# Kernel tuning notes

Measured on AMD Instinct MI355X. Metric: run time of the kernel, lower is better.

## Reference

```python
import jax, jax.numpy as jnp
import numpy as np

B, T, L, D, U = 2048, 500, 128, 64, 128  # batch, time steps, latent_dim, output_dim, n_units


def setup_inputs() -> dict:
    key = jax.random.key(0)
    ks = jax.random.split(key, 10)
    def init(k, shape, fan_in):
        return jax.random.uniform(k, shape, jnp.float32, -1.0, 1.0) / np.sqrt(fan_in)
    return {
        "first_point": jax.random.normal(ks[0], (1, B, L), jnp.float32),
        "time_steps_to_predict": jnp.arange(T, dtype=jnp.float32),
        # GRUCell params (torch layout: weight [3*hidden, in], gates ordered r,z,n)
        "w_ih": init(ks[1], (3 * L, D + 1), L),
        "w_hh": init(ks[2], (3 * L, L), L),
        "b_ih": init(ks[3], (3 * L,), L),
        "b_hh": init(ks[4], (3 * L,), L),
        # output_net: Linear(L,U) -> tanh -> Linear(U,D)
        "w1": init(ks[5], (U, L), L),
        "b1": jnp.zeros((U,), jnp.float32),
        "w2": init(ks[6], (D, U), U),
        "b2": jnp.zeros((D,), jnp.float32),
    }


def _gru_cell(x, h, w_ih, w_hh, b_ih, b_hh):
    gi = x @ w_ih.T + b_ih  # [B, 3L]
    gh = h @ w_hh.T + b_hh  # [B, 3L]
    i_r, i_z, i_n = jnp.split(gi, 3, axis=-1)
    h_r, h_z, h_n = jnp.split(gh, 3, axis=-1)
    r = jax.nn.sigmoid(i_r + h_r)
    z = jax.nn.sigmoid(i_z + h_z)
    n = jnp.tanh(i_n + r * h_n)
    return (1.0 - z) * n + z * h


def reference(first_point, time_steps_to_predict, w_ih, w_hh, b_ih, b_hh, w1, b1, w2, b2):
    def mlp(h):
        return jnp.tanh(h @ w1.T + b1) @ w2.T + b2  # [B, D]

    ts = time_steps_to_predict
    delta_ts = jnp.concatenate([jnp.zeros((1,), ts.dtype), ts[1:] - ts[:-1]])  # [T]

    h0 = first_point[0]          # [B, L]
    p0 = mlp(h0)                 # [B, D]
    batch = h0.shape[0]

    def step(carry, dt):
        h, p = carry
        dt_col = jnp.broadcast_to(dt.reshape(1, 1), (batch, 1))
        x = jnp.concatenate([p, dt_col], axis=-1)  # [B, D+1]
        h = _gru_cell(x, h, w_ih, w_hh, b_ih, b_hh)
        p = mlp(h)
        return (h, p), (h, p)

    _, (hs, ps) = jax.lax.scan(step, (h0, p0), delta_ts[1:])  # [T-1, B, *]
    sol_z = jnp.concatenate([h0[None], hs], axis=0)   # [T, B, L]
    pred_x = jnp.concatenate([p0[None], ps], axis=0)  # [T, B, D]
    sol_z = jnp.transpose(sol_z, (1, 0, 2))[None]     # [1, B, T, L]
    pred_x = jnp.transpose(pred_x, (1, 0, 2))[None]   # [1, B, T, D]
    return sol_z, pred_x
```

## Files before the change

### kernel.cpp

```cpp
#include <hip/hip_runtime.h>

#define BB 2048
#define TT 500
#define LL 128
#define DD 64
#define UU 128

using f16x8 = __attribute__((ext_vector_type(8))) _Float16;
using f32x4 = __attribute__((ext_vector_type(4))) float;

__device__ __forceinline__ float bf2f(unsigned short u){
  union { unsigned u; float f; } v; v.u = ((unsigned)u) << 16; return v.f;
}
__device__ __forceinline__ unsigned short f2bf(float f){
  union { float f; unsigned u; } v; v.f = f;
  unsigned r = v.u + 0x7FFFu + ((v.u >> 16) & 1u);
  return (unsigned short)(r >> 16);
}
__device__ __forceinline__ float cvt(unsigned short v){ return bf2f(v); }
__device__ __forceinline__ float cvt(float v){ return v; }

__device__ __forceinline__ float sigmoidf_(float x){
  return __builtin_amdgcn_rcpf(1.f + __expf(-x));
}
__device__ __forceinline__ float tanhf_(float x){
  float e = __expf(2.f * x);
  return 1.f - 2.f * __builtin_amdgcn_rcpf(1.f + e);
}

#define SH 136
#define SP 72
#define SA 136

struct Frags {
  f16x8 Wp[3][2];
  f16x8 Wh[3][4];
  f16x8 W1f[4];
  f16x8 W2f[4];
  float br, bz, bin, bhn, wdr, wdz, wdn, b1c, b2c;
};

template <typename T>
__device__ __forceinline__ void preload(
    const void* wih_, const void* whh_, const void* bih_, const void* bhh_,
    const void* w1_, const void* b1_, const void* w2_, const void* b2_,
    int c, int lq, Frags& F)
{
  const T* wih = (const T*)wih_; const T* whh = (const T*)whh_;
  const T* bih = (const T*)bih_; const T* bhh = (const T*)bhh_;
  const T* w1  = (const T*)w1_;  const T* b1  = (const T*)b1_;
  const T* w2  = (const T*)w2_;  const T* b2  = (const T*)b2_;
  #pragma unroll
  for (int g = 0; g < 3; ++g){
    const int row = g*128 + c;
    #pragma unroll
    for (int kt = 0; kt < 2; ++kt)
      #pragma unroll
      for (int j = 0; j < 8; ++j)
        F.Wp[g][kt][j] = (_Float16)cvt(wih[row*65 + kt*32 + lq*8 + j]);
    #pragma unroll
    for (int kt = 0; kt < 4; ++kt)
      #pragma unroll
      for (int j = 0; j < 8; ++j)
        F.Wh[g][kt][j] = (_Float16)cvt(whh[row*128 + kt*32 + lq*8 + j]);
  }
  #pragma unroll
  for (int kt = 0; kt < 4; ++kt)
    #pragma unroll
    for (int j = 0; j < 8; ++j)
      F.W1f[kt][j] = (_Float16)cvt(w1[c*128 + kt*32 + lq*8 + j]);
  const int c2 = c & 63;
  #pragma unroll
  for (int kt = 0; kt < 4; ++kt)
    #pragma unroll
    for (int j = 0; j < 8; ++j)
      F.W2f[kt][j] = (_Float16)cvt(w2[c2*128 + kt*32 + lq*8 + j]);
  F.br  = cvt(bih[c])     + cvt(bhh[c]);
  F.bz  = cvt(bih[128+c]) + cvt(bhh[128+c]);
  F.bin = cvt(bih[256+c]);
  F.bhn = cvt(bhh[256+c]);
  F.wdr = cvt(wih[c*65 + 64]);
  F.wdz = cvt(wih[(128+c)*65 + 64]);
  F.wdn = cvt(wih[(256+c)*65 + 64]);
  F.b1c = cvt(b1[c]);
  F.b2c = cvt(b2[c2]);
}

__global__ __launch_bounds__(512, 2) void rnn_decoder(
    const void* __restrict__ fp0,
    const void* __restrict__ ts,
    const void* __restrict__ wih,
    const void* __restrict__ whh,
    const void* __restrict__ bih,
    const void* __restrict__ bhh,
    const void* __restrict__ w1,
    const void* __restrict__ b1,
    const void* __restrict__ w2,
    const void* __restrict__ b2,
    void* __restrict__ out)
{
  __shared__ __align__(16) _Float16 sh[16*SH];
  __shared__ __align__(16) _Float16 sp[16*SP];
  __shared__ __align__(16) _Float16 sa[16*SA];
  __shared__ float dts[TT];

  const int tid  = threadIdx.x;
  const int wv   = tid >> 6;
  const int lane = tid & 63;
  const int lm   = lane & 15;
  const int lq   = lane >> 4;
  const int b0   = blockIdx.x << 4;
  const int c    = (wv << 4) + lm;

  const bool isbf = (((const unsigned*)ts)[1] != 0x3F800000u);

  for (int i = tid; i < 16*SH; i += 512) sh[i] = (_Float16)0.f;
  for (int i = tid; i < 16*SP; i += 512) sp[i] = (_Float16)0.f;
  for (int i = tid; i < 16*SA; i += 512) sa[i] = (_Float16)0.f;

  Frags F;
  if (isbf) preload<unsigned short>(wih, whh, bih, bhh, w1, b1, w2, b2, c, lq, F);
  else      preload<float>         (wih, whh, bih, bhh, w1, b1, w2, b2, c, lq, F);

  if (isbf){
    const unsigned short* t16 = (const unsigned short*)ts;
    for (int t = tid; t < TT; t += 512)
      dts[t] = t ? (bf2f(t16[t]) - bf2f(t16[t-1])) : 0.f;
  } else {
    const float* t32 = (const float*)ts;
    for (int t = tid; t < TT; t += 512)
      dts[t] = t ? (t32[t] - t32[t-1]) : 0.f;
  }

  {
    const int row = tid >> 5;
    const int k4  = (tid & 31) << 2;
    if (isbf){
      const unsigned short* src = (const unsigned short*)fp0 + (b0 + row)*LL + k4;
      #pragma unroll
      for (int j = 0; j < 4; ++j) sh[row*SH + k4 + j] = (_Float16)bf2f(src[j]);
    } else {
      const float* src = (const float*)fp0 + (b0 + row)*LL + k4;
      #pragma unroll
      for (int j = 0; j < 4; ++j) sh[row*SH + k4 + j] = (_Float16)src[j];
    }
  }
  __syncthreads();

  float hprev[4];
  #pragma unroll
  for (int i = 0; i < 4; ++i)
    hprev[i] = (float)sh[(lq*4 + i)*SH + c];

  unsigned short* outh16 = (unsigned short*)out;
  unsigned short* outp16 = outh16 + (size_t)BB*TT*LL;
  float* outh32 = (float*)out;
  float* outp32 = outh32 + (size_t)BB*TT*LL;

  for (int t = 0; t < TT; ++t){
    if (t > 0){
      const float dt = dts[t];
      f16x8 ap[2], ah[4];
      #pragma unroll
      for (int kt = 0; kt < 2; ++kt)
        ap[kt] = *(const f16x8*)&sp[lm*SP + kt*32 + lq*8];
      #pragma unroll
      for (int kt = 0; kt < 4; ++kt)
        ah[kt] = *(const f16x8*)&sh[lm*SH + kt*32 + lq*8];
      f32x4 aR = {0,0,0,0}, aZ = {0,0,0,0}, aN = {0,0,0,0}, aH = {0,0,0,0};
      #pragma unroll
      for (int kt = 0; kt < 2; ++kt){
        aR = __builtin_amdgcn_mfma_f32_16x16x32_f16(ap[kt], F.Wp[0][kt], aR, 0,0,0);
        aZ = __builtin_amdgcn_mfma_f32_16x16x32_f16(ap[kt], F.Wp[1][kt], aZ, 0,0,0);
        aN = __builtin_amdgcn_mfma_f32_16x16x32_f16(ap[kt], F.Wp[2][kt], aN, 0,0,0);
      }
      #pragma unroll
      for (int kt = 0; kt < 4; ++kt){
        aR = __builtin_amdgcn_mfma_f32_16x16x32_f16(ah[kt], F.Wh[0][kt], aR, 0,0,0);
        aZ = __builtin_amdgcn_mfma_f32_16x16x32_f16(ah[kt], F.Wh[1][kt], aZ, 0,0,0);
        aH = __builtin_amdgcn_mfma_f32_16x16x32_f16(ah[kt], F.Wh[2][kt], aH, 0,0,0);
      }
      float hnew[4];
      #pragma unroll
      for (int i = 0; i < 4; ++i){
        const float r = sigmoidf_(aR[i] + F.br + dt*F.wdr);
        const float z = sigmoidf_(aZ[i] + F.bz + dt*F.wdz);
        const float n = tanhf_(aN[i] + F.bin + dt*F.wdn + r*(aH[i] + F.bhn));
        hnew[i] = (1.f - z)*n + z*hprev[i];
        hprev[i] = hnew[i];
      }
      __syncthreads();
      #pragma unroll
      for (int i = 0; i < 4; ++i)
        sh[(lq*4 + i)*SH + c] = (_Float16)hnew[i];
      __syncthreads();
    }
    {
      f16x8 ahm[4];
      #pragma unroll
      for (int kt = 0; kt < 4; ++kt)
        ahm[kt] = *(const f16x8*)&sh[lm*SH + kt*32 + lq*8];
      f32x4 acc = {0,0,0,0};
      #pragma unroll
      for (int kt = 0; kt < 4; ++kt)
        acc = __builtin_amdgcn_mfma_f32_16x16x32_f16(ahm[kt], F.W1f[kt], acc, 0,0,0);
      #pragma unroll
      for (int i = 0; i < 4; ++i)
        sa[(lq*4 + i)*SA + c] = (_Float16)tanhf_(acc[i] + F.b1c);
    }
    __syncthreads();
    if (wv < 4){
      f16x8 aam[4];
      #pragma unroll
      for (int kt = 0; kt < 4; ++kt)
        aam[kt] = *(const f16x8*)&sa[lm*SA + kt*32 + lq*8];
      f32x4 acc = {0,0,0,0};
      #pragma unroll
      for (int kt = 0; kt < 4; ++kt)
        acc = __builtin_amdgcn_mfma_f32_16x16x32_f16(aam[kt], F.W2f[kt], acc, 0,0,0);
      #pragma unroll
      for (int i = 0; i < 4; ++i)
        sp[(lq*4 + i)*SP + c] = (_Float16)(acc[i] + F.b2c);
    }
    __syncthreads();
    {
      const int row = tid >> 5;
      const size_t hb = (size_t)(b0 + row)*TT + t;
      const int k4 = (tid & 31) << 2;
      const int k2 = (tid & 31) << 1;
      if (isbf){
        ushort4 hv;
        hv.x = f2bf((float)sh[row*SH + k4 + 0]);
        hv.y = f2bf((float)sh[row*SH + k4 + 1]);
        hv.z = f2bf((float)sh[row*SH + k4 + 2]);
        hv.w = f2bf((float)sh[row*SH + k4 + 3]);
        *(ushort4*)(outh16 + hb*LL + k4) = hv;
        ushort2 pv;
        pv.x = f2bf((float)sp[row*SP + k2 + 0]);
        pv.y = f2bf((float)sp[row*SP + k2 + 1]);
        *(ushort2*)(outp16 + hb*DD + k2) = pv;
      } else {
        float4 hv;
        hv.x = (float)sh[row*SH + k4 + 0];
        hv.y = (float)sh[row*SH + k4 + 1];
        hv.z = (float)sh[row*SH + k4 + 2];
        hv.w = (float)sh[row*SH + k4 + 3];
        *(float4*)(outh32 + hb*LL + k4) = hv;
        float2 pv;
        pv.x = (float)sp[row*SP + k2 + 0];
        pv.y = (float)sp[row*SP + k2 + 1];
        *(float2*)(outp32 + hb*DD + k2) = pv;
      }
    }
  }
}

extern "C" void kernel_launch(void* const* d_in, const int* in_sizes, int n_in,
                              void* d_out, int out_size, void* d_ws, size_t ws_size,
                              hipStream_t stream) {
  (void)in_sizes; (void)n_in; (void)out_size; (void)d_ws; (void)ws_size;
  rnn_decoder<<<dim3(BB/16), dim3(512), 0, stream>>>(
      d_in[0],
      d_in[1],
      d_in[2],
      d_in[3],
      d_in[4],
      d_in[5],
      d_in[6],
      d_in[7],
      d_in[8],
      d_in[9],
      d_out);
}
```

Baseline: 1.444 ms.

## Fold output projection into GRU input weights and write outputs directly from registers

Precomputes Wc = W_ih[:, :64] @ W2 and a folded bias so the GRU input gates take the tanh activation directly, dropping the p staging buffer and one barrier phase per step. The p output is computed alongside the gates, off the critical path. h and p are now stored straight from MFMA registers to global memory instead of being re-read from shared memory. Costs are an O(64) per-thread prologue loop, extra MFMAs per step (K=128 instead of 64 for the input part), and scattered element-wise global stores that replace the vectorized ones.

```diff
diff --git a/kernel.cpp b/kernel.cpp
--- a/kernel.cpp
+++ b/kernel.cpp
@@ -29,11 +29,10 @@
 }
 
 #define SH 136
-#define SP 72
 #define SA 136
 
 struct Frags {
-  f16x8 Wp[3][2];
+  f16x8 Wc[3][4];
   f16x8 Wh[3][4];
   f16x8 W1f[4];
   f16x8 W2f[4];
@@ -54,11 +53,6 @@
   for (int g = 0; g < 3; ++g){
     const int row = g*128 + c;
     #pragma unroll
-    for (int kt = 0; kt < 2; ++kt)
-      #pragma unroll
-      for (int j = 0; j < 8; ++j)
-        F.Wp[g][kt][j] = (_Float16)cvt(wih[row*65 + kt*32 + lq*8 + j]);
-    #pragma unroll
     for (int kt = 0; kt < 4; ++kt)
       #pragma unroll
       for (int j = 0; j < 8; ++j)
@@ -75,9 +69,41 @@
     #pragma unroll
     for (int j = 0; j < 8; ++j)
       F.W2f[kt][j] = (_Float16)cvt(w2[c2*128 + kt*32 + lq*8 + j]);
-  F.br  = cvt(bih[c])     + cvt(bhh[c]);
-  F.bz  = cvt(bih[128+c]) + cvt(bhh[128+c]);
-  F.bin = cvt(bih[256+c]);
+
+  for (int kt = 0; kt < 4; ++kt){
+    float acc[3][8];
+    #pragma unroll
+    for (int g = 0; g < 3; ++g)
+      #pragma unroll
+      for (int j = 0; j < 8; ++j) acc[g][j] = 0.f;
+    for (int d = 0; d < 64; ++d){
+      float w2r[8];
+      #pragma unroll
+      for (int j = 0; j < 8; ++j)
+        w2r[j] = cvt(w2[d*128 + kt*32 + lq*8 + j]);
+      #pragma unroll
+      for (int g = 0; g < 3; ++g){
+        const float wpv = cvt(wih[(g*128 + c)*65 + d]);
+        #pragma unroll
+        for (int j = 0; j < 8; ++j) acc[g][j] += wpv * w2r[j];
+      }
+    }
+    #pragma unroll
+    for (int g = 0; g < 3; ++g)
+      #pragma unroll
+      for (int j = 0; j < 8; ++j)
+        F.Wc[g][kt][j] = (_Float16)acc[g][j];
+  }
+  float bc[3] = {0.f, 0.f, 0.f};
+  for (int d = 0; d < 64; ++d){
+    const float b2v = cvt(b2[d]);
+    #pragma unroll
+    for (int g = 0; g < 3; ++g)
+      bc[g] += cvt(wih[(g*128 + c)*65 + d]) * b2v;
+  }
+  F.br  = cvt(bih[c])     + cvt(bhh[c])     + bc[0];
+  F.bz  = cvt(bih[128+c]) + cvt(bhh[128+c]) + bc[1];
+  F.bin = cvt(bih[256+c]) + bc[2];
   F.bhn = cvt(bhh[256+c]);
   F.wdr = cvt(wih[c*65 + 64]);
   F.wdz = cvt(wih[(128+c)*65 + 64]);
@@ -100,7 +126,6 @@
     void* __restrict__ out)
 {
   __shared__ __align__(16) _Float16 sh[16*SH];
-  __shared__ __align__(16) _Float16 sp[16*SP];
   __shared__ __align__(16) _Float16 sa[16*SA];
   __shared__ float dts[TT];
 
@@ -113,10 +138,6 @@
   const int c    = (wv << 4) + lm;
 
   const bool isbf = (((const unsigned*)ts)[1] != 0x3F800000u);
-
-  for (int i = tid; i < 16*SH; i += 512) sh[i] = (_Float16)0.f;
-  for (int i = tid; i < 16*SP; i += 512) sp[i] = (_Float16)0.f;
-  for (int i = tid; i < 16*SA; i += 512) sa[i] = (_Float16)0.f;
 
   Frags F;
   if (isbf) preload<unsigned short>(wih, whh, bih, bhh, w1, b1, w2, b2, c, lq, F);
@@ -132,17 +153,29 @@
       dts[t] = t ? (t32[t] - t32[t-1]) : 0.f;
   }
 
+  unsigned short* outh16 = (unsigned short*)out;
+  unsigned short* outp16 = outh16 + (size_t)BB*TT*LL;
+  float* outh32 = (float*)out;
+  float* outp32 = outh32 + (size_t)BB*TT*LL;
+
   {
     const int row = tid >> 5;
     const int k4  = (tid & 31) << 2;
     if (isbf){
       const unsigned short* src = (const unsigned short*)fp0 + (b0 + row)*LL + k4;
-      #pragma unroll
-      for (int j = 0; j < 4; ++j) sh[row*SH + k4 + j] = (_Float16)bf2f(src[j]);
+      ushort4 v = *(const ushort4*)src;
+      #pragma unroll
+      for (int j = 0; j < 4; ++j)
+        sh[row*SH + k4 + j] = (_Float16)bf2f(((const unsigned short*)&v)[j]);
+      *(ushort4*)(outh16 + (size_t)(b0 + row)*TT*LL + k4) = v;
     } else {
       const float* src = (const float*)fp0 + (b0 + row)*LL + k4;
-      #pragma unroll
-      for (int j = 0; j < 4; ++j) sh[row*SH + k4 + j] = (_Float16)src[j];
+      float4 v = *(const float4*)src;
+      sh[row*SH + k4 + 0] = (_Float16)v.x;
+      sh[row*SH + k4 + 1] = (_Float16)v.y;
+      sh[row*SH + k4 + 2] = (_Float16)v.z;
+      sh[row*SH + k4 + 3] = (_Float16)v.w;
+      *(float4*)(outh32 + (size_t)(b0 + row)*TT*LL + k4) = v;
     }
   }
   __syncthreads();
@@ -152,105 +185,109 @@
   for (int i = 0; i < 4; ++i)
     hprev[i] = (float)sh[(lq*4 + i)*SH + c];
 
-  unsigned short* outh16 = (unsigned short*)out;
-  unsigned short* outp16 = outh16 + (size_t)BB*TT*LL;
-  float* outh32 = (float*)out;
-  float* outp32 = outh32 + (size_t)BB*TT*LL;
-
-  for (int t = 0; t < TT; ++t){
-    if (t > 0){
-      const float dt = dts[t];
-      f16x8 ap[2], ah[4];
-      #pragma unroll
-      for (int kt = 0; kt < 2; ++kt)
-        ap[kt] = *(const f16x8*)&sp[lm*SP + kt*32 + lq*8];
+  f16x8 ahc[4], aac[4];
+  #pragma unroll
+  for (int kt = 0; kt < 4; ++kt)
+    ahc[kt] = *(const f16x8*)&sh[lm*SH + kt*32 + lq*8];
+
+  {
+    f32x4 acc = {0,0,0,0};
+    #pragma unroll
+    for (int kt = 0; kt < 4; ++kt)
+      acc = __builtin_amdgcn_mfma_f32_16x16x32_f16(ahc[kt], F.W1f[kt], acc, 0,0,0);
+    #pragma unroll
+    for (int i = 0; i < 4; ++i)
+      sa[(lq*4 + i)*SA + c] = (_Float16)tanhf_(acc[i] + F.b1c);
+  }
+  __syncthreads();
+  #pragma unroll
+  for (int kt = 0; kt < 4; ++kt)
+    aac[kt] = *(const f16x8*)&sa[lm*SA + kt*32 + lq*8];
+
+  for (int t = 1; t < TT; ++t){
+    const float dt = dts[t];
+    f32x4 aR = {0,0,0,0}, aZ = {0,0,0,0}, aN = {0,0,0,0}, aH = {0,0,0,0};
+    #pragma unroll
+    for (int kt = 0; kt < 4; ++kt){
+      aR = __builtin_amdgcn_mfma_f32_16x16x32_f16(aac[kt], F.Wc[0][kt], aR, 0,0,0);
+      aZ = __builtin_amdgcn_mfma_f32_16x16x32_f16(aac[kt], F.Wc[1][kt], aZ, 0,0,0);
+      aN = __builtin_amdgcn_mfma_f32_16x16x32_f16(aac[kt], F.Wc[2][kt], aN, 0,0,0);
+      aH = __builtin_amdgcn_mfma_f32_16x16x32_f16(ahc[kt], F.Wh[2][kt], aH, 0,0,0);
+    }
+    #pragma unroll
+    for (int kt = 0; kt < 4; ++kt){
+      aR = __builtin_amdgcn_mfma_f32_16x16x32_f16(ahc[kt], F.Wh[0][kt], aR, 0,0,0);
+      aZ = __builtin_amdgcn_mfma_f32_16x16x32_f16(ahc[kt], F.Wh[1][kt], aZ, 0,0,0);
+    }
+    f32x4 aP = {0,0,0,0};
+    if (wv < 4){
       #pragma unroll
       for (int kt = 0; kt < 4; ++kt)
-        ah[kt] = *(const f16x8*)&sh[lm*SH + kt*32 + lq*8];
-      f32x4 aR = {0,0,0,0}, aZ = {0,0,0,0}, aN = {0,0,0,0}, aH = {0,0,0,0};
-      #pragma unroll
-      for (int kt = 0; kt < 2; ++kt){
-        aR = __builtin_amdgcn_mfma_f32_16x16x32_f16(ap[kt], F.Wp[0][kt], aR, 0,0,0);
-        aZ = __builtin_amdgcn_mfma_f32_16x16x32_f16(ap[kt], F.Wp[1][kt], aZ, 0,0,0);
-        aN = __builtin_amdgcn_mfma_f32_16x16x32_f16(ap[kt], F.Wp[2][kt], aN, 0,0,0);
+        aP = __builtin_amdgcn_mfma_f32_16x16x32_f16(aac[kt], F.W2f[kt], aP, 0,0,0);
+    }
+    float hnew[4];
+    #pragma unroll
+    for (int i = 0; i < 4; ++i){
+      const float r = sigmoidf_(aR[i] + F.br + dt*F.wdr);
+      const float z = sigmoidf_(aZ[i] + F.bz + dt*F.wdz);
+      const float n = tanhf_(aN[i] + F.bin + dt*F.wdn + r*(aH[i] + F.bhn));
+      hnew[i] = (1.f - z)*n + z*hprev[i];
+      hprev[i] = hnew[i];
+    }
+    #pragma unroll
+    for (int i = 0; i < 4; ++i)
+      sh[(lq*4 + i)*SH + c] = (_Float16)hnew[i];
+    if (!isbf){
+      #pragma unroll
+      for (int i = 0; i < 4; ++i)
+        outh32[(size_t)(b0 + lq*4 + i)*TT*LL + (size_t)t*LL + c] = hnew[i];
+      if (wv < 4){
+        #pragma unroll
+        for (int i = 0; i < 4; ++i)
+          outp32[(size_t)(b0 + lq*4 + i)*TT*DD + (size_t)(t-1)*DD + c] = aP[i] + F.b2c;
       }
-      #pragma unroll
-      for (int kt = 0; kt < 4; ++kt){
-        aR = __builtin_amdgcn_mfma_f32_16x16x32_f16(ah[kt], F.Wh[0][kt], aR, 0,0,0);
-        aZ = __builtin_amdgcn_mfma_f32_16x16x32_f16(ah[kt], F.Wh[1][kt], aZ, 0,0,0);
-        aH = __builtin_amdgcn_mfma_f32_16x16x32_f16(ah[kt], F.Wh[2][kt], aH, 0,0,0);
+    } else {
+      #pragma unroll
+      for (int i = 0; i < 4; ++i)
+        outh16[(size_t)(b0 + lq*4 + i)*TT*LL + (size_t)t*LL + c] = f2bf(hnew[i]);
+      if (wv < 4){
+        #pragma unroll
+        for (int i = 0; i < 4; ++i)
+          outp16[(size_t)(b0 + lq*4 + i)*TT*DD + (size_t)(t-1)*DD + c] = f2bf(aP[i] + F.b2c);
       }
-      float hnew[4];
-      #pragma unroll
-      for (int i = 0; i < 4; ++i){
-        const float r = sigmoidf_(aR[i] + F.br + dt*F.wdr);
-        const float z = sigmoidf_(aZ[i] + F.bz + dt*F.wdz);
-        const float n = tanhf_(aN[i] + F.bin + dt*F.wdn + r*(aH[i] + F.bhn));
-        hnew[i] = (1.f - z)*n + z*hprev[i];
-        hprev[i] = hnew[i];
-      }
-      __syncthreads();
-      #pragma unroll
-      for (int i = 0; i < 4; ++i)
-        sh[(lq*4 + i)*SH + c] = (_Float16)hnew[i];
-      __syncthreads();
-    }
+    }
+    __syncthreads();
+    #pragma unroll
+    for (int kt = 0; kt < 4; ++kt)
+      ahc[kt] = *(const f16x8*)&sh[lm*SH + kt*32 + lq*8];
     {
-      f16x8 ahm[4];
+      f32x4 acc = {0,0,0,0};
       #pragma unroll
       for (int kt = 0; kt < 4; ++kt)
-        ahm[kt] = *(const f16x8*)&sh[lm*SH + kt*32 + lq*8];
-      f32x4 acc = {0,0,0,0};
-      #pragma unroll
-      for (int kt = 0; kt < 4; ++kt)
-        acc = __builtin_amdgcn_mfma_f32_16x16x32_f16(ahm[kt], F.W1f[kt], acc, 0,0,0);
+        acc = __builtin_amdgcn_mfma_f32_16x16x32_f16(ahc[kt], F.W1f[kt], acc, 0,0,0);
       #pragma unroll
       for (int i = 0; i < 4; ++i)
         sa[(lq*4 + i)*SA + c] = (_Float16)tanhf_(acc[i] + F.b1c);
     }
     __syncthreads();
-    if (wv < 4){
-      f16x8 aam[4];
-      #pragma unroll
-      for (int kt = 0; kt < 4; ++kt)
-        aam[kt] = *(const f16x8*)&sa[lm*SA + kt*32 + lq*8];
-      f32x4 acc = {0,0,0,0};
-      #pragma unroll
-      for (int kt = 0; kt < 4; ++kt)
-        acc = __builtin_amdgcn_mfma_f32_16x16x32_f16(aam[kt], F.W2f[kt], acc, 0,0,0);
-      #pragma unroll
-      for (int i = 0; i < 4; ++i)
-        sp[(lq*4 + i)*SP + c] = (_Float16)(acc[i] + F.b2c);
-    }
-    __syncthreads();
-    {
-      const int row = tid >> 5;
-      const size_t hb = (size_t)(b0 + row)*TT + t;
-      const int k4 = (tid & 31) << 2;
-      const int k2 = (tid & 31) << 1;
-      if (isbf){
-        ushort4 hv;
-        hv.x = f2bf((float)sh[row*SH + k4 + 0]);
-        hv.y = f2bf((float)sh[row*SH + k4 + 1]);
-        hv.z = f2bf((float)sh[row*SH + k4 + 2]);
-        hv.w = f2bf((float)sh[row*SH + k4 + 3]);
-        *(ushort4*)(outh16 + hb*LL + k4) = hv;
-        ushort2 pv;
-        pv.x = f2bf((float)sp[row*SP + k2 + 0]);
-        pv.y = f2bf((float)sp[row*SP + k2 + 1]);
-        *(ushort2*)(outp16 + hb*DD + k2) = pv;
-      } else {
-        float4 hv;
-        hv.x = (float)sh[row*SH + k4 + 0];
-        hv.y = (float)sh[row*SH + k4 + 1];
-        hv.z = (float)sh[row*SH + k4 + 2];
-        hv.w = (float)sh[row*SH + k4 + 3];
-        *(float4*)(outh32 + hb*LL + k4) = hv;
-        float2 pv;
-        pv.x = (float)sp[row*SP + k2 + 0];
-        pv.y = (float)sp[row*SP + k2 + 1];
-        *(float2*)(outp32 + hb*DD + k2) = pv;
-      }
+    #pragma unroll
+    for (int kt = 0; kt < 4; ++kt)
+      aac[kt] = *(const f16x8*)&sa[lm*SA + kt*32 + lq*8];
+  }
+
+  if (wv < 4){
+    f32x4 aP = {0,0,0,0};
+    #pragma unroll
+    for (int kt = 0; kt < 4; ++kt)
+      aP = __builtin_amdgcn_mfma_f32_16x16x32_f16(aac[kt], F.W2f[kt], aP, 0,0,0);
+    if (!isbf){
+      #pragma unroll
+      for (int i = 0; i < 4; ++i)
+        outp32[(size_t)(b0 + lq*4 + i)*TT*DD + (size_t)(TT-1)*DD + c] = aP[i] + F.b2c;
+    } else {
+      #pragma unroll
+      for (int i = 0; i < 4; ++i)
+        outp16[(size_t)(b0 + lq*4 + i)*TT*DD + (size_t)(TT-1)*DD + c] = f2bf(aP[i] + F.b2c);
     }
   }
 }
```

Measured after the change: 1.330 ms. 1.09x faster.
